# Performance work log

Measured on AMD Instinct MI355X. Metric: run time of the kernel, lower is better.

## Reference

```python
import jax, jax.numpy as jnp
import numpy as np

INP = 512
HIDDEN = 512
N_HEADS = 8          # called 'head_dim' in the torch code
D_HEAD = HIDDEN // N_HEADS  # 64
BASE = 10000.0
SCALE = D_HEAD ** (-0.5)


def rope(x):
    # x: [b, s, h, d]
    b, s, h, d = x.shape
    half = d // 2
    theta = 1.0 / (BASE ** (jnp.arange(0, d, 2, dtype=jnp.float32) / d))  # [d/2]
    idx_theta = jnp.arange(s, dtype=jnp.float32)[:, None] * theta[None, :]  # [s, d/2]
    idx_theta2 = jnp.concatenate([idx_theta, idx_theta], axis=1)            # [s, d]
    neg_half = jnp.concatenate([-x[..., half:], x[..., :half]], axis=-1)
    cos = jnp.cos(idx_theta2)[None, :, None, :]
    sin = jnp.sin(idx_theta2)[None, :, None, :]
    return x * cos + neg_half * sin


def setup_inputs() -> dict:
    key = jax.random.key(0)
    ks = jax.random.split(key, 10)
    b, s = 4, 2048
    init = lambda k, shp, fan_in: jax.random.normal(k, shp, jnp.float32) * (fan_in ** -0.5)
    return {
        "x": jax.random.normal(ks[0], (b, s, INP), jnp.float32),
        "c": jax.random.normal(ks[1], (b, s, INP), jnp.float32),
        "Wq": init(ks[2], (INP, HIDDEN), INP), "bq": jnp.zeros((HIDDEN,), jnp.float32),
        "Wk": init(ks[3], (INP, HIDDEN), INP), "bk": jnp.zeros((HIDDEN,), jnp.float32),
        "Wv": init(ks[4], (INP, HIDDEN), INP), "bv": jnp.zeros((HIDDEN,), jnp.float32),
        "Wo": init(ks[5], (HIDDEN, INP), HIDDEN), "bo": jnp.zeros((INP,), jnp.float32),
    }


def reference(x, c, Wq, bq, Wk, bk, Wv, bv, Wo, bo):
    b, s, _ = x.shape
    h_res = x
    q = (c @ Wq + bq).reshape(b, s, N_HEADS, D_HEAD)
    k = (x @ Wk + bk).reshape(b, s, N_HEADS, D_HEAD)
    v = (x @ Wv + bv).reshape(b, s, N_HEADS, D_HEAD)
    q = rope(q)
    k = rope(k)  # computed but unused, exactly as in the source
    # NOTE: source computes scores between q and V (not k) -- faithful reproduction
    att = jnp.einsum('bihd,bjhd->bhij', q, v)            # [b, h, s, s]
    att = jax.nn.softmax(att * SCALE, axis=-1)
    out = jnp.einsum('bhij,bjhd->bihd', att, v)          # [b, s, h, d]
    out = out.reshape(b, s, HIDDEN)
    out = out @ Wo + bo
    return out + h_res
```

## Files before the change

kernel.cpp:

```cpp
#include <hip/hip_runtime.h>
#include <hip/hip_bf16.h>
#include <cstdint>

typedef float f32x4 __attribute__((ext_vector_type(4)));
typedef float f32x16 __attribute__((ext_vector_type(16)));
typedef short bf16x8 __attribute__((ext_vector_type(8)));
typedef short bf16x4 __attribute__((ext_vector_type(4)));
typedef unsigned int u32x2 __attribute__((ext_vector_type(2)));
typedef unsigned short u16;

#define B_    4
#define S_    2048
#define H_    8
#define D_    64
#define M_    8192

#define OFF_CBF   0UL
#define OFF_XBF   8388608UL
#define OFF_QBH   16777216UL
#define OFF_VBH   25165824UL
#define OFF_VTBH  33554432UL
#define OFF_ATTN  41943040UL
#define OFF_WQT   50331648UL
#define OFF_WVT   50855936UL
#define OFF_WOT   51380224UL
#define OFF_BIAS  51904512UL
#define OFF_COS   51910656UL
#define OFF_SIN   52172800UL
#define WS_NEEDED 52434944UL

__device__ __forceinline__ u16 f2bf(float f){
    union { float f; uint32_t u; } v; v.f = f;
    uint32_t r = (v.u + 0x7fffu + ((v.u >> 16) & 1u)) >> 16;
    return (u16)r;
}
__device__ __forceinline__ float bf2f(u16 h){
    union { uint32_t u; float f; } v; v.u = ((uint32_t)h) << 16;
    return v.f;
}

__device__ __forceinline__ uint32_t cvtpk(float lo, float hi){
    uint32_t r;
    asm("v_cvt_pk_bf16_f32 %0, %1, %2" : "=v"(r) : "v"(lo), "v"(hi));
    return r;
}
__device__ __forceinline__ void plswap(uint32_t &va, uint32_t &vb){
#if __has_builtin(__builtin_amdgcn_permlane32_swap)
    u32x2 r = __builtin_amdgcn_permlane32_swap(va, vb, false, false);
    va = r[0]; vb = r[1];
#else
    asm volatile("v_permlane32_swap_b32 %0, %1" : "+v"(va), "+v"(vb));
#endif
}

__device__ __forceinline__ f32x16 mfma32(bf16x8 a, bf16x8 b, f32x16 c){
    return __builtin_amdgcn_mfma_f32_32x32x16_bf16(a, b, c, 0, 0, 0);
}

__device__ __forceinline__ void deint(uint4 a, uint4 b, bf16x8 &lo, bf16x8 &hi){
    union { bf16x8 v; uint32_t d[4]; } L, H;
    uint32_t s0=a.x, s1=a.y, s2=a.z, s3=a.w, s4=b.x, s5=b.y, s6=b.z, s7=b.w;
    L.d[0] = (s0 & 0xffffu) | (s1 << 16);
    L.d[1] = (s2 & 0xffffu) | (s3 << 16);
    L.d[2] = (s4 & 0xffffu) | (s5 << 16);
    L.d[3] = (s6 & 0xffffu) | (s7 << 16);
    H.d[0] = (s0 >> 16) | (s1 & 0xffff0000u);
    H.d[1] = (s2 >> 16) | (s3 & 0xffff0000u);
    H.d[2] = (s4 >> 16) | (s5 & 0xffff0000u);
    H.d[3] = (s6 >> 16) | (s7 & 0xffff0000u);
    lo = L.v; hi = H.v;
}

__device__ __forceinline__ int swz(int row, int col){
    return (col & ~63) | ((((col >> 3) & 7) ^ (row & 7)) << 3) | (col & 7);
}

__device__ __forceinline__ int detect_f32(const void* x_in){
    int lane = threadIdx.x & 63;
    ushort2 dv = ((const ushort2*)x_in)[lane];
    bool hit = ((((dv.x >> 7) & 0xFF) >= 160) || (((dv.y >> 7) & 0xFF) >= 160));
    return __ballot(hit) != 0ULL;
}

__device__ __forceinline__ void gload_lds16(const u16* g, u16* l){
    __builtin_amdgcn_global_load_lds(
        (const __attribute__((address_space(1))) void*)g,
        (__attribute__((address_space(3))) void*)l, 16, 0, 0);
}

__global__ void k_prep(const void* c_in, const void* x_in,
                       const void* Wq, const void* Wv, const void* Wo,
                       const void* bq, const void* bv, const void* bo,
                       u16* c_bf, u16* x_bf,
                       u16* Wqt, u16* Wvt, u16* Wot, float* bias_ws,
                       float* cos_t, float* sin_t){
    int bid = blockIdx.x;
    if (bid >= 7168){
        int idx = (bid - 7168) * 256 + threadIdx.x;
        int pos = idx >> 5, j = idx & 31;
        double theta = pow(10000.0, -(double)j / 32.0);
        double rev = ((double)pos * theta) * 0.15915494309189535;
        rev -= floor(rev);
        float fr = (float)rev;
        cos_t[idx] = __builtin_amdgcn_cosf(fr);
        sin_t[idx] = __builtin_amdgcn_sinf(fr);
        return;
    }
    if (bid >= 4096){
        int f = detect_f32(x_in);
        int wi = (bid - 4096) >> 10;
        int idx = ((bid - 4096) & 1023) * 256 + threadIdx.x;
        int k = idx >> 9, n = idx & 511;
        const void* W; u16* Wt; const void* bb;
        if (wi == 0){ W = Wq; Wt = Wqt; bb = bq; }
        else if (wi == 1){ W = Wv; Wt = Wvt; bb = bv; }
        else { W = Wo; Wt = Wot; bb = bo; }
        float v = f ? ((const float*)W)[idx] : bf2f(((const u16*)W)[idx]);
        Wt[n * 512 + (wi == 2 ? k : swz(n, k))] = f2bf(v);
        if (idx < 512){
            float b = f ? ((const float*)bb)[idx] : bf2f(((const u16*)bb)[idx]);
            bias_ws[wi * 512 + idx] = b;
        }
        return;
    }
    int f = detect_f32(x_in);
    int isx = bid >= 2048;
    int t = (bid & 2047) * 256 + threadIdx.x;
    const void* src = isx ? x_in : c_in;
    u16* dst = isx ? x_bf : c_bf;
    int e0 = t * 8, row = e0 >> 9, col = e0 & 511;
    size_t didx = (size_t)row * 512 + swz(row, col);
    bf16x8 o;
    if (f){
        float4 lo = ((const float4*)src)[t*2];
        float4 hi = ((const float4*)src)[t*2 + 1];
        union { bf16x8 v; uint32_t d[4]; } u;
        u.d[0] = cvtpk(lo.x, lo.y); u.d[1] = cvtpk(lo.z, lo.w);
        u.d[2] = cvtpk(hi.x, hi.y); u.d[3] = cvtpk(hi.z, hi.w);
        o = u.v;
    } else {
        o = *(const bf16x8*)((const u16*)src + e0);
    }
    *(bf16x8*)(dst + didx) = o;
}

__global__ __launch_bounds__(256) void k_gemm_qv(
    const u16* __restrict__ c_bf, const u16* __restrict__ x_bf,
    const u16* __restrict__ Wqt, const u16* __restrict__ Wvt,
    const float* __restrict__ bias_ws,
    const float* __restrict__ cos_t, const float* __restrict__ sin_t,
    u16* __restrict__ Qbh, u16* __restrict__ Vbh, u16* __restrict__ Vtbh)
{
    __shared__ __align__(16) u16 Als[2][128 * 64];
    __shared__ __align__(16) u16 Bls[2][128 * 64];
    const int w = threadIdx.x >> 6, lane = threadIdx.x & 63;
    const int g = lane >> 4, cq = lane & 15;
    const int wm = w & 1, wn = w >> 1;
    const int z = blockIdx.z;
    const u16* A  = z ? x_bf : c_bf;
    const u16* Wt = z ? Wvt : Wqt;
    const float* bias = bias_ws + (z ? 512 : 0);
    const int m0b = blockIdx.x * 128, n0b = blockIdx.y * 128;
    const int m0 = m0b + wm * 64, n0 = n0b + wn * 64;
    const int swzi = ((cq & 7) << 3);

    int srow[4], scol[4];
    #pragma unroll
    for (int i = 0; i < 4; i++){
        int flat = (w * 4 + i) * 64 + lane;
        srow[i] = flat >> 3; scol[i] = (flat & 7) * 8;
    }

    const f32x4 zero = {0.f, 0.f, 0.f, 0.f};
    f32x4 acc[4][4];
    #pragma unroll
    for (int i = 0; i < 4; i++)
        #pragma unroll
        for (int j = 0; j < 4; j++) acc[i][j] = zero;

    #pragma unroll
    for (int i = 0; i < 4; i++){
        gload_lds16(A  + (size_t)(m0b + srow[i]) * 512 + scol[i], &Als[0][(w*4 + i) * 512]);
        gload_lds16(Wt + (size_t)(n0b + srow[i]) * 512 + scol[i], &Bls[0][(w*4 + i) * 512]);
    }

    for (int kt = 0; kt < 8; kt++){
        const int buf = kt & 1;
        __builtin_amdgcn_s_waitcnt(0x0F70);
        __syncthreads();
        if (kt < 7){
            const int kk = (kt + 1) * 64;
            #pragma unroll
            for (int i = 0; i < 4; i++){
                gload_lds16(A  + (size_t)(m0b + srow[i]) * 512 + kk + scol[i], &Als[buf^1][(w*4 + i) * 512]);
                gload_lds16(Wt + (size_t)(n0b + srow[i]) * 512 + kk + scol[i], &Bls[buf^1][(w*4 + i) * 512]);
            }
        }
        #pragma unroll
        for (int ks = 0; ks < 2; ks++){
            const int cs = ((ks * 4 + g) << 3) ^ swzi;
            bf16x8 a[4], b[4];
            #pragma unroll
            for (int mt = 0; mt < 4; mt++)
                a[mt] = *(const bf16x8*)&Als[buf][(wm*64 + mt*16 + cq) * 64 + cs];
            #pragma unroll
            for (int nt = 0; nt < 4; nt++)
                b[nt] = *(const bf16x8*)&Bls[buf][(wn*64 + nt*16 + cq) * 64 + cs];
            #pragma unroll
            for (int mt = 0; mt < 4; mt++)
                #pragma unroll
                for (int nt = 0; nt < 4; nt++)
                    acc[mt][nt] = __builtin_amdgcn_mfma_f32_16x16x32_bf16(a[mt], b[nt], acc[mt][nt], 0, 0, 0);
        }
    }
    __syncthreads();

    #pragma unroll
    for (int nt = 0; nt < 4; nt++){
        float bvv = bias[n0 + nt*16 + cq];
        #pragma unroll
        for (int mt = 0; mt < 4; mt++) acc[mt][nt] += bvv;
    }
    const int h = n0 >> 6;
    if (z == 0){
        const float SCL = 0.125f * 1.4426950408889634f;
        uint32_t* Qpk = (uint32_t*)Qbh;
        #pragma unroll
        for (int mt = 0; mt < 4; mt++){
            #pragma unroll
            for (int r = 0; r < 4; r++){
                int row = m0 + mt*16 + g*4 + r;
                int b_idx = row >> 11, si = row & 2047;
                size_t base = ((size_t)(b_idx*8 + h) * 2048 + si) * 32;
                #pragma unroll
                for (int nt = 0; nt < 2; nt++){
                    int dj = nt*16 + cq;
                    float cv = cos_t[si*32 + dj], sv = sin_t[si*32 + dj];
                    float x1 = acc[mt][nt][r], x2 = acc[mt][nt+2][r];
                    Qpk[base + dj] = cvtpk((x1*cv - x2*sv) * SCL, (x2*cv + x1*sv) * SCL);
                }
            }
        }
    } else {
        float* ltw = ((float*)&Als[0][0]) + w * (16 * 65);
        const int b_idx = m0 >> 11, si0 = m0 & 2047;
        const size_t tbase = ((size_t)(b_idx*8 + h) * 64) * 2048;
        #pragma unroll
        for (int mt = 0; mt < 4; mt++)
            #pragma unroll
            for (int r = 0; r < 4; r++){
                int row = m0 + mt*16 + g*4 + r;
                int bi = row >> 11, si = row & 2047;
                size_t base = ((size_t)(bi*8 + h) * 2048 + si) * 64;
                #pragma unroll
                for (int nt = 0; nt < 4; nt++)
                    Vbh[base + nt*16 + cq] = f2bf(acc[mt][nt][r]);
            }
        #pragma unroll
        for (int nt = 0; nt < 4; nt++){
            #pragma unroll
            for (int mt = 0; mt < 4; mt++)
                #pragma unroll
                for (int r = 0; r < 4; r++)
                    ltw[cq * 65 + mt*16 + g*4 + r] = acc[mt][nt][r];
            __builtin_amdgcn_wave_barrier();
            #pragma unroll
            for (int dd = 0; dd < 16; dd++){
                float v = ltw[dd * 65 + lane];
                Vtbh[tbase + (size_t)(nt*16 + dd) * 2048 + si0 + lane] = f2bf(v);
            }
            __builtin_amdgcn_wave_barrier();
        }
    }
}

__global__ __launch_bounds__(256, 2) void k_attn(
    const u16* __restrict__ Qbh, const u16* __restrict__ Vbh,
    const u16* __restrict__ Vtbh,
    u16* __restrict__ part0, u16* __restrict__ part1, float* __restrict__ lsum)
{
    __shared__ __align__(16) u16 Vs[2][64 * 68];
    __shared__ __align__(16) u16 Vts[2][64 * 68];

    const int bid = blockIdx.x;
    const int logical = (bid & 7) * 64 + (bid >> 3);
    const int xb = logical & 7;
    const int bh = (logical >> 3) & 31;
    const int z  = logical >> 8;

    const int w = threadIdx.x >> 6, lane = threadIdx.x & 63;
    const int r32 = lane & 31, hl = lane >> 5;
    const int i0 = xb * 256 + w * 64;
    const int j0 = z * 1024;

    const uint32_t* Qpk = (const uint32_t*)Qbh;
    bf16x8 aq[2][4];
    #pragma unroll
    for (int it = 0; it < 2; it++){
        size_t qb = ((size_t)bh*2048 + i0 + it*32 + r32)*32 + hl*8;
        uint4 a0 = *(const uint4*)&Qpk[qb];
        uint4 a1 = *(const uint4*)&Qpk[qb + 4];
        uint4 b0 = *(const uint4*)&Qpk[qb + 16];
        uint4 b1 = *(const uint4*)&Qpk[qb + 20];
        deint(a0, a1, aq[it][0], aq[it][2]);
        deint(b0, b1, aq[it][1], aq[it][3]);
    }

    const int sr = w * 16 + (lane >> 2), sc = (lane & 3) * 16;
    const u16* gvs = Vbh  + ((size_t)bh*2048 + j0 + sr) * 64 + sc;
    const u16* gvt = Vtbh + ((size_t)bh*64 + sr) * 2048 + j0 + sc;
    const int ls = sr * 68 + sc;

    {
        bf16x8 a0 = *(const bf16x8*)gvs,       a1 = *(const bf16x8*)(gvs + 8);
        bf16x8 b0 = *(const bf16x8*)gvt,       b1 = *(const bf16x8*)(gvt + 8);
        *(bf16x8*)&Vs[0][ls]  = a0;  *(bf16x8*)&Vs[0][ls + 8]  = a1;
        *(bf16x8*)&Vts[0][ls] = b0;  *(bf16x8*)&Vts[0][ls + 8] = b1;
    }

    f32x16 ot[2][2];
    #pragma unroll
    for (int it = 0; it < 2; it++)
        #pragma unroll
        for (int dt = 0; dt < 2; dt++)
            #pragma unroll
            for (int rr = 0; rr < 16; rr++) ot[it][dt][rr] = 0.f;
    const f32x16 zero16 = ot[0][0];
    float fl[2] = {0.f, 0.f};
    bf16x8 pb[2][4];

    {
        bf16x8 na0 = *(const bf16x8*)(gvs + 4096);
        bf16x8 na1 = *(const bf16x8*)(gvs + 4096 + 8);
        bf16x8 nb0 = *(const bf16x8*)(gvt + 64);
        bf16x8 nb1 = *(const bf16x8*)(gvt + 64 + 8);
        __syncthreads();
        #pragma unroll
        for (int jtile = 0; jtile < 2; jtile++){
            bf16x8 vf[4];
            #pragma unroll
            for (int kk = 0; kk < 4; kk++)
                vf[kk] = *(const bf16x8*)&Vs[0][(jtile*32 + r32)*68 + kk*16 + hl*8];
            f32x16 st0 = zero16, st1 = zero16;
            __builtin_amdgcn_s_setprio(1);
            #pragma unroll
            for (int kk = 0; kk < 4; kk++){
                st0 = mfma32(vf[kk], aq[0][kk], st0);
                st1 = mfma32(vf[kk], aq[1][kk], st1);
            }
            __builtin_amdgcn_s_setprio(0);
            #pragma unroll
            for (int rr = 0; rr < 16; rr++) st0[rr] = __builtin_amdgcn_exp2f(st0[rr]);
            #pragma unroll
            for (int rr = 0; rr < 16; rr++) st1[rr] = __builtin_amdgcn_exp2f(st1[rr]);
            fl[0] += ((st0[0]+st0[1])+(st0[2]+st0[3])) + ((st0[4]+st0[5])+(st0[6]+st0[7]))
                   + ((st0[8]+st0[9])+(st0[10]+st0[11])) + ((st0[12]+st0[13])+(st0[14]+st0[15]));
            fl[1] += ((st1[0]+st1[1])+(st1[2]+st1[3])) + ((st1[4]+st1[5])+(st1[6]+st1[7]))
                   + ((st1[8]+st1[9])+(st1[10]+st1[11])) + ((st1[12]+st1[13])+(st1[14]+st1[15]));
            #pragma unroll
            for (int c = 0; c < 2; c++){
                uint32_t dA1 = cvtpk(st0[c*8+0], st0[c*8+1]);
                uint32_t dA2 = cvtpk(st0[c*8+2], st0[c*8+3]);
                uint32_t dB1 = cvtpk(st0[c*8+4], st0[c*8+5]);
                uint32_t dB2 = cvtpk(st0[c*8+6], st0[c*8+7]);
                plswap(dA1, dB1); plswap(dA2, dB2);
                union { bf16x8 v; uint32_t d[4]; } u;
                u.d[0] = dA1; u.d[1] = dA2; u.d[2] = dB1; u.d[3] = dB2;
                pb[0][jtile*2 + c] = u.v;
            }
            #pragma unroll
            for (int c = 0; c < 2; c++){
                uint32_t dA1 = cvtpk(st1[c*8+0], st1[c*8+1]);
                uint32_t dA2 = cvtpk(st1[c*8+2], st1[c*8+3]);
                uint32_t dB1 = cvtpk(st1[c*8+4], st1[c*8+5]);
                uint32_t dB2 = cvtpk(st1[c*8+6], st1[c*8+7]);
                plswap(dA1, dB1); plswap(dA2, dB2);
                union { bf16x8 v; uint32_t d[4]; } u;
                u.d[0] = dA1; u.d[1] = dA2; u.d[2] = dB1; u.d[3] = dB2;
                pb[1][jtile*2 + c] = u.v;
            }
        }
        *(bf16x8*)&Vs[1][ls]  = na0;  *(bf16x8*)&Vs[1][ls + 8]  = na1;
        *(bf16x8*)&Vts[1][ls] = nb0;  *(bf16x8*)&Vts[1][ls + 8] = nb1;
    }

    for (int jt = 1; jt < 16; jt++){
        const int bufA = jt & 1, bufB = bufA ^ 1;
        __syncthreads();
        bf16x8 na0, na1, nb0, nb1;
        if (jt < 15){
            na0 = *(const bf16x8*)(gvs + (size_t)(jt + 1) * 4096);
            na1 = *(const bf16x8*)(gvs + (size_t)(jt + 1) * 4096 + 8);
            nb0 = *(const bf16x8*)(gvt + (size_t)(jt + 1) * 64);
            nb1 = *(const bf16x8*)(gvt + (size_t)(jt + 1) * 64 + 8);
        }
        #pragma unroll
        for (int jtile = 0; jtile < 2; jtile++){
            bf16x8 vf[4];
            #pragma unroll
            for (int kk = 0; kk < 4; kk++)
                vf[kk] = *(const bf16x8*)&Vs[bufA][(jtile*32 + r32)*68 + kk*16 + hl*8];
            f32x16 st0 = zero16, st1 = zero16;
            __builtin_amdgcn_s_setprio(1);
            #pragma unroll
            for (int kk = 0; kk < 4; kk++){
                st0 = mfma32(vf[kk], aq[0][kk], st0);
                st1 = mfma32(vf[kk], aq[1][kk], st1);
            }
            #pragma unroll
            for (int cc = 0; cc < 2; cc++){
                const int c = jtile*2 + cc;
                bf16x8 vt0 = *(const bf16x8*)&Vts[bufB][r32*68 + c*16 + hl*8];
                bf16x8 vt1 = *(const bf16x8*)&Vts[bufB][(32 + r32)*68 + c*16 + hl*8];
                ot[0][0] = mfma32(vt0, pb[0][c], ot[0][0]);
                ot[1][0] = mfma32(vt0, pb[1][c], ot[1][0]);
                ot[0][1] = mfma32(vt1, pb[0][c], ot[0][1]);
                ot[1][1] = mfma32(vt1, pb[1][c], ot[1][1]);
            }
            __builtin_amdgcn_s_setprio(0);
            #pragma unroll
            for (int rr = 0; rr < 16; rr++) st0[rr] = __builtin_amdgcn_exp2f(st0[rr]);
            #pragma unroll
            for (int rr = 0; rr < 16; rr++) st1[rr] = __builtin_amdgcn_exp2f(st1[rr]);
            fl[0] += ((st0[0]+st0[1])+(st0[2]+st0[3])) + ((st0[4]+st0[5])+(st0[6]+st0[7]))
                   + ((st0[8]+st0[9])+(st0[10]+st0[11])) + ((st0[12]+st0[13])+(st0[14]+st0[15]));
            fl[1] += ((st1[0]+st1[1])+(st1[2]+st1[3])) + ((st1[4]+st1[5])+(st1[6]+st1[7]))
                   + ((st1[8]+st1[9])+(st1[10]+st1[11])) + ((st1[12]+st1[13])+(st1[14]+st1[15]));
            #pragma unroll
            for (int c = 0; c < 2; c++){
                uint32_t dA1 = cvtpk(st0[c*8+0], st0[c*8+1]);
                uint32_t dA2 = cvtpk(st0[c*8+2], st0[c*8+3]);
                uint32_t dB1 = cvtpk(st0[c*8+4], st0[c*8+5]);
                uint32_t dB2 = cvtpk(st0[c*8+6], st0[c*8+7]);
                plswap(dA1, dB1); plswap(dA2, dB2);
                union { bf16x8 v; uint32_t d[4]; } u;
                u.d[0] = dA1; u.d[1] = dA2; u.d[2] = dB1; u.d[3] = dB2;
                pb[0][jtile*2 + c] = u.v;
            }
            #pragma unroll
            for (int c = 0; c < 2; c++){
                uint32_t dA1 = cvtpk(st1[c*8+0], st1[c*8+1]);
                uint32_t dA2 = cvtpk(st1[c*8+2], st1[c*8+3]);
                uint32_t dB1 = cvtpk(st1[c*8+4], st1[c*8+5]);
                uint32_t dB2 = cvtpk(st1[c*8+6], st1[c*8+7]);
                plswap(dA1, dB1); plswap(dA2, dB2);
                union { bf16x8 v; uint32_t d[4]; } u;
                u.d[0] = dA1; u.d[1] = dA2; u.d[2] = dB1; u.d[3] = dB2;
                pb[1][jtile*2 + c] = u.v;
            }
        }
        __syncthreads();
        if (jt < 15){
            *(bf16x8*)&Vs[bufB][ls]  = na0;  *(bf16x8*)&Vs[bufB][ls + 8]  = na1;
            *(bf16x8*)&Vts[bufB][ls] = nb0;  *(bf16x8*)&Vts[bufB][ls + 8] = nb1;
        }
    }

    __builtin_amdgcn_s_setprio(1);
    #pragma unroll
    for (int c = 0; c < 4; c++){
        bf16x8 vt0 = *(const bf16x8*)&Vts[1][r32*68 + c*16 + hl*8];
        bf16x8 vt1 = *(const bf16x8*)&Vts[1][(32 + r32)*68 + c*16 + hl*8];
        ot[0][0] = mfma32(vt0, pb[0][c], ot[0][0]);
        ot[1][0] = mfma32(vt0, pb[1][c], ot[1][0]);
        ot[0][1] = mfma32(vt1, pb[0][c], ot[0][1]);
        ot[1][1] = mfma32(vt1, pb[1][c], ot[1][1]);
    }
    __builtin_amdgcn_s_setprio(0);

    const int b_idx = bh >> 3, hh = bh & 7;
    u16* part = z ? part1 : part0;
    #pragma unroll
    for (int it = 0; it < 2; it++){
        float sum = fl[it] + __shfl_xor(fl[it], 32);
        const int row = b_idx*2048 + i0 + it*32 + r32;
        if (lane < 32)
            lsum[(size_t)z*65536 + (size_t)hh*8192 + row] = sum;
        #pragma unroll
        for (int dt = 0; dt < 2; dt++){
            #pragma unroll
            for (int q = 0; q < 4; q++){
                float v0 = ot[it][dt][q*4+0];
                float v1 = ot[it][dt][q*4+1];
                float v2 = ot[it][dt][q*4+2];
                float v3 = ot[it][dt][q*4+3];
                uint2 pw;
                pw.x = cvtpk(v0, v1);
                pw.y = cvtpk(v2, v3);
                int col = hh*64 + dt*32 + q*8 + hl*4;
                *(uint2*)&part[(size_t)row * 512 + col] = pw;
            }
        }
    }
}

__global__ __launch_bounds__(256) void k_gemm_out(
    const u16* __restrict__ part0, const u16* __restrict__ part1,
    const float* __restrict__ lsum,
    const u16* __restrict__ Wot, const float* __restrict__ bias_ws,
    const void* __restrict__ x_in, void* __restrict__ out)
{
    __shared__ __align__(16) u16 Als[2][128 * 68];
    __shared__ __align__(16) u16 Bls[2][64 * 68];
    const int w = threadIdx.x >> 6, lane = threadIdx.x & 63;
    const int g = lane >> 4, cq = lane & 15;
    const int wm = w & 1, wn = w >> 1;
    const int m0b = blockIdx.x * 128, n0b = blockIdx.y * 64;
    const int m0 = m0b + wm * 64, n0 = n0b + wn * 32;
    const int f = detect_f32(x_in);

    int sra[4], sca[4], srb[2], scb[2];
    #pragma unroll
    for (int i = 0; i < 4; i++){
        int flat = (w * 4 + i) * 64 + lane;
        sra[i] = flat >> 3; sca[i] = (flat & 7) * 8;
    }
    #pragma unroll
    for (int i = 0; i < 2; i++){
        int flat = (w * 2 + i) * 64 + lane;
        srb[i] = flat >> 3; scb[i] = (flat & 7) * 8;
    }

    const f32x4 zero = {0.f, 0.f, 0.f, 0.f};
    f32x4 acc[4][2];
    #pragma unroll
    for (int i = 0; i < 4; i++)
        #pragma unroll
        for (int j = 0; j < 2; j++) acc[i][j] = zero;

    bf16x8 pa0[4], pa1[4], pb[2]; float pr[4];
    #pragma unroll
    for (int i = 0; i < 4; i++){
        int row = m0b + sra[i];
        pa0[i] = *(const bf16x8*)&part0[(size_t)row * 512 + sca[i]];
        pa1[i] = *(const bf16x8*)&part1[(size_t)row * 512 + sca[i]];
        pr[i] = 1.f / (lsum[row] + lsum[65536 + row]);
    }
    #pragma unroll
    for (int i = 0; i < 2; i++)
        pb[i] = *(const bf16x8*)&Wot[(size_t)(n0b + srb[i]) * 512 + scb[i]];
    #pragma unroll
    for (int i = 0; i < 4; i++){
        union { bf16x8 v; u16 e[8]; } a8;
        #pragma unroll
        for (int e = 0; e < 8; e++)
            a8.e[e] = f2bf((bf2f((u16)pa0[i][e]) + bf2f((u16)pa1[i][e])) * pr[i]);
        *(bf16x8*)&Als[0][sra[i]*68 + sca[i]] = a8.v;
    }
    #pragma unroll
    for (int i = 0; i < 2; i++)
        *(bf16x8*)&Bls[0][srb[i]*68 + scb[i]] = pb[i];

    for (int kt = 0; kt < 8; kt++){
        const int buf = kt & 1;
        __syncthreads();
        if (kt < 7){
            const int kk = (kt + 1) * 64, h = kt + 1;
            #pragma unroll
            for (int i = 0; i < 4; i++){
                int row = m0b + sra[i];
                pa0[i] = *(const bf16x8*)&part0[(size_t)row * 512 + kk + sca[i]];
                pa1[i] = *(const bf16x8*)&part1[(size_t)row * 512 + kk + sca[i]];
                pr[i] = 1.f / (lsum[(size_t)h*8192 + row] + lsum[65536 + (size_t)h*8192 + row]);
            }
            #pragma unroll
            for (int i = 0; i < 2; i++)
                pb[i] = *(const bf16x8*)&Wot[(size_t)(n0b + srb[i]) * 512 + kk + scb[i]];
        }
        #pragma unroll
        for (int ks = 0; ks < 2; ks++){
            bf16x8 a[4], b[2];
            #pragma unroll
            for (int mt = 0; mt < 4; mt++)
                a[mt] = *(const bf16x8*)&Als[buf][(wm*64 + mt*16 + cq)*68 + ks*32 + g*8];
            #pragma unroll
            for (int nt = 0; nt < 2; nt++)
                b[nt] = *(const bf16x8*)&Bls[buf][(wn*32 + nt*16 + cq)*68 + ks*32 + g*8];
            #pragma unroll
            for (int mt = 0; mt < 4; mt++)
                #pragma unroll
                for (int nt = 0; nt < 2; nt++)
                    acc[mt][nt] = __builtin_amdgcn_mfma_f32_16x16x32_bf16(a[mt], b[nt], acc[mt][nt], 0, 0, 0);
        }
        if (kt < 7){
            #pragma unroll
            for (int i = 0; i < 4; i++){
                union { bf16x8 v; u16 e[8]; } a8;
                #pragma unroll
                for (int e = 0; e < 8; e++)
                    a8.e[e] = f2bf((bf2f((u16)pa0[i][e]) + bf2f((u16)pa1[i][e])) * pr[i]);
                *(bf16x8*)&Als[buf^1][sra[i]*68 + sca[i]] = a8.v;
            }
            #pragma unroll
            for (int i = 0; i < 2; i++)
                *(bf16x8*)&Bls[buf^1][srb[i]*68 + scb[i]] = pb[i];
        }
    }
    #pragma unroll
    for (int mt = 0; mt < 4; mt++)
        #pragma unroll
        for (int nt = 0; nt < 2; nt++)
            #pragma unroll
            for (int r = 0; r < 4; r++){
                int row = m0 + mt*16 + g*4 + r;
                int col = n0 + nt*16 + cq;
                size_t idx = (size_t)row * 512 + col;
                float resid = f ? ((const float*)x_in)[idx] : bf2f(((const u16*)x_in)[idx]);
                float v = acc[mt][nt][r] + bias_ws[1024 + col] + resid;
                if (f) ((float*)out)[idx] = v;
                else   ((u16*)out)[idx] = f2bf(v);
            }
}

extern "C" void kernel_launch(void* const* d_in, const int* in_sizes, int n_in,
                              void* d_out, int out_size, void* d_ws, size_t ws_size,
                              hipStream_t stream){
    const void* x_in = d_in[0];
    const void* c_in = d_in[1];
    const void* Wq = d_in[2]; const void* bq = d_in[3];
    const void* Wv = d_in[6]; const void* bv = d_in[7];
    const void* Wo = d_in[8]; const void* bo = d_in[9];

    if (ws_size < WS_NEEDED){
        hipMemsetAsync(d_out, 0, (size_t)out_size * 2, stream);
        return;
    }
    char* ws = (char*)d_ws;
    u16* c_bf  = (u16*)(ws + OFF_CBF);
    u16* x_bf  = (u16*)(ws + OFF_XBF);
    u16* Qbh   = (u16*)(ws + OFF_QBH);
    u16* Vbh   = (u16*)(ws + OFF_VBH);
    u16* Vtbh  = (u16*)(ws + OFF_VTBH);
    u16* part0 = (u16*)(ws + OFF_ATTN);
    u16* part1 = (u16*)(ws + OFF_CBF);
    float* lsum = (float*)(ws + OFF_XBF);
    u16* Wqt   = (u16*)(ws + OFF_WQT);
    u16* Wvt   = (u16*)(ws + OFF_WVT);
    u16* Wot   = (u16*)(ws + OFF_WOT);
    float* bias_ws = (float*)(ws + OFF_BIAS);
    float* cos_t   = (float*)(ws + OFF_COS);
    float* sin_t   = (float*)(ws + OFF_SIN);

    k_prep<<<7424, 256, 0, stream>>>(c_in, x_in, Wq, Wv, Wo, bq, bv, bo,
                                     c_bf, x_bf, Wqt, Wvt, Wot, bias_ws, cos_t, sin_t);
    k_gemm_qv<<<dim3(64, 4, 2), 256, 0, stream>>>(c_bf, x_bf, Wqt, Wvt, bias_ws,
                                                  cos_t, sin_t, Qbh, Vbh, Vtbh);
    k_attn<<<dim3(512), 256, 0, stream>>>(Qbh, Vbh, Vtbh, part0, part1, lsum);
    k_gemm_out<<<dim3(64, 8), 256, 0, stream>>>(part0, part1, lsum, Wot, bias_ws,
                                                x_in, d_out);
}
```

Measured before the change: 181.7 us.

## Halve attention query rows per wave and double grid for occupancy

```diff
diff --git a/kernel.cpp b/kernel.cpp
--- a/kernel.cpp
+++ b/kernel.cpp
@@ -274,7 +274,7 @@
     }
 }
 
-__global__ __launch_bounds__(256, 2) void k_attn(
+__global__ __launch_bounds__(256, 4) void k_attn(
     const u16* __restrict__ Qbh, const u16* __restrict__ Vbh,
     const u16* __restrict__ Vtbh,
     u16* __restrict__ part0, u16* __restrict__ part1, float* __restrict__ lsum)
@@ -283,27 +283,26 @@
     __shared__ __align__(16) u16 Vts[2][64 * 68];
 
     const int bid = blockIdx.x;
-    const int logical = (bid & 7) * 64 + (bid >> 3);
-    const int xb = logical & 7;
-    const int bh = (logical >> 3) & 31;
-    const int z  = logical >> 8;
+    const int logical = (bid & 7) * 128 + (bid >> 3);
+    const int xb = logical & 15;
+    const int bh = (logical >> 4) & 31;
+    const int z  = logical >> 9;
 
     const int w = threadIdx.x >> 6, lane = threadIdx.x & 63;
     const int r32 = lane & 31, hl = lane >> 5;
-    const int i0 = xb * 256 + w * 64;
+    const int i0 = xb * 128 + w * 32;
     const int j0 = z * 1024;
 
     const uint32_t* Qpk = (const uint32_t*)Qbh;
-    bf16x8 aq[2][4];
-    #pragma unroll
-    for (int it = 0; it < 2; it++){
-        size_t qb = ((size_t)bh*2048 + i0 + it*32 + r32)*32 + hl*8;
+    bf16x8 aq[4];
+    {
+        size_t qb = ((size_t)bh*2048 + i0 + r32)*32 + hl*8;
         uint4 a0 = *(const uint4*)&Qpk[qb];
         uint4 a1 = *(const uint4*)&Qpk[qb + 4];
         uint4 b0 = *(const uint4*)&Qpk[qb + 16];
         uint4 b1 = *(const uint4*)&Qpk[qb + 20];
-        deint(a0, a1, aq[it][0], aq[it][2]);
-        deint(b0, b1, aq[it][1], aq[it][3]);
+        deint(a0, a1, aq[0], aq[2]);
+        deint(b0, b1, aq[1], aq[3]);
     }
 
     const int sr = w * 16 + (lane >> 2), sc = (lane & 3) * 16;
@@ -318,16 +317,14 @@
         *(bf16x8*)&Vts[0][ls] = b0;  *(bf16x8*)&Vts[0][ls + 8] = b1;
     }
 
-    f32x16 ot[2][2];
-    #pragma unroll
-    for (int it = 0; it < 2; it++)
-        #pragma unroll
-        for (int dt = 0; dt < 2; dt++)
-            #pragma unroll
-            for (int rr = 0; rr < 16; rr++) ot[it][dt][rr] = 0.f;
-    const f32x16 zero16 = ot[0][0];
-    float fl[2] = {0.f, 0.f};
-    bf16x8 pb[2][4];
+    f32x16 ot[2];
+    #pragma unroll
+    for (int dt = 0; dt < 2; dt++)
+        #pragma unroll
+        for (int rr = 0; rr < 16; rr++) ot[dt][rr] = 0.f;
+    const f32x16 zero16 = ot[0];
+    float fl = 0.f;
+    bf16x8 pb[4];
 
     {
         bf16x8 na0 = *(const bf16x8*)(gvs + 4096);
@@ -341,43 +338,26 @@
             #pragma unroll
             for (int kk = 0; kk < 4; kk++)
                 vf[kk] = *(const bf16x8*)&Vs[0][(jtile*32 + r32)*68 + kk*16 + hl*8];
-            f32x16 st0 = zero16, st1 = zero16;
+            f32x16 st = zero16;
             __builtin_amdgcn_s_setprio(1);
             #pragma unroll
-            for (int kk = 0; kk < 4; kk++){
-                st0 = mfma32(vf[kk], aq[0][kk], st0);
-                st1 = mfma32(vf[kk], aq[1][kk], st1);
-            }
+            for (int kk = 0; kk < 4; kk++)
+                st = mfma32(vf[kk], aq[kk], st);
             __builtin_amdgcn_s_setprio(0);
             #pragma unroll
-            for (int rr = 0; rr < 16; rr++) st0[rr] = __builtin_amdgcn_exp2f(st0[rr]);
-            #pragma unroll
-            for (int rr = 0; rr < 16; rr++) st1[rr] = __builtin_amdgcn_exp2f(st1[rr]);
-            fl[0] += ((st0[0]+st0[1])+(st0[2]+st0[3])) + ((st0[4]+st0[5])+(st0[6]+st0[7]))
-                   + ((st0[8]+st0[9])+(st0[10]+st0[11])) + ((st0[12]+st0[13])+(st0[14]+st0[15]));
-            fl[1] += ((st1[0]+st1[1])+(st1[2]+st1[3])) + ((st1[4]+st1[5])+(st1[6]+st1[7]))
-                   + ((st1[8]+st1[9])+(st1[10]+st1[11])) + ((st1[12]+st1[13])+(st1[14]+st1[15]));
+            for (int rr = 0; rr < 16; rr++) st[rr] = __builtin_amdgcn_exp2f(st[rr]);
+            fl += ((st[0]+st[1])+(st[2]+st[3])) + ((st[4]+st[5])+(st[6]+st[7]))
+                + ((st[8]+st[9])+(st[10]+st[11])) + ((st[12]+st[13])+(st[14]+st[15]));
             #pragma unroll
             for (int c = 0; c < 2; c++){
-                uint32_t dA1 = cvtpk(st0[c*8+0], st0[c*8+1]);
-                uint32_t dA2 = cvtpk(st0[c*8+2], st0[c*8+3]);
-                uint32_t dB1 = cvtpk(st0[c*8+4], st0[c*8+5]);
-                uint32_t dB2 = cvtpk(st0[c*8+6], st0[c*8+7]);
+                uint32_t dA1 = cvtpk(st[c*8+0], st[c*8+1]);
+                uint32_t dA2 = cvtpk(st[c*8+2], st[c*8+3]);
+                uint32_t dB1 = cvtpk(st[c*8+4], st[c*8+5]);
+                uint32_t dB2 = cvtpk(st[c*8+6], st[c*8+7]);
                 plswap(dA1, dB1); plswap(dA2, dB2);
                 union { bf16x8 v; uint32_t d[4]; } u;
                 u.d[0] = dA1; u.d[1] = dA2; u.d[2] = dB1; u.d[3] = dB2;
-                pb[0][jtile*2 + c] = u.v;
-            }
-            #pragma unroll
-            for (int c = 0; c < 2; c++){
-                uint32_t dA1 = cvtpk(st1[c*8+0], st1[c*8+1]);
-                uint32_t dA2 = cvtpk(st1[c*8+2], st1[c*8+3]);
-                uint32_t dB1 = cvtpk(st1[c*8+4], st1[c*8+5]);
-                uint32_t dB2 = cvtpk(st1[c*8+6], st1[c*8+7]);
-                plswap(dA1, dB1); plswap(dA2, dB2);
-                union { bf16x8 v; uint32_t d[4]; } u;
-                u.d[0] = dA1; u.d[1] = dA2; u.d[2] = dB1; u.d[3] = dB2;
-                pb[1][jtile*2 + c] = u.v;
+                pb[jtile*2 + c] = u.v;
             }
         }
         *(bf16x8*)&Vs[1][ls]  = na0;  *(bf16x8*)&Vs[1][ls + 8]  = na1;
@@ -400,53 +380,34 @@
             #pragma unroll
             for (int kk = 0; kk < 4; kk++)
                 vf[kk] = *(const bf16x8*)&Vs[bufA][(jtile*32 + r32)*68 + kk*16 + hl*8];
-            f32x16 st0 = zero16, st1 = zero16;
+            f32x16 st = zero16;
             __builtin_amdgcn_s_setprio(1);
             #pragma unroll
-            for (int kk = 0; kk < 4; kk++){
-                st0 = mfma32(vf[kk], aq[0][kk], st0);
-                st1 = mfma32(vf[kk], aq[1][kk], st1);
-            }
+            for (int kk = 0; kk < 4; kk++)
+                st = mfma32(vf[kk], aq[kk], st);
             #pragma unroll
             for (int cc = 0; cc < 2; cc++){
                 const int c = jtile*2 + cc;
                 bf16x8 vt0 = *(const bf16x8*)&Vts[bufB][r32*68 + c*16 + hl*8];
                 bf16x8 vt1 = *(const bf16x8*)&Vts[bufB][(32 + r32)*68 + c*16 + hl*8];
-                ot[0][0] = mfma32(vt0, pb[0][c], ot[0][0]);
-                ot[1][0] = mfma32(vt0, pb[1][c], ot[1][0]);
-                ot[0][1] = mfma32(vt1, pb[0][c], ot[0][1]);
-                ot[1][1] = mfma32(vt1, pb[1][c], ot[1][1]);
+                ot[0] = mfma32(vt0, pb[c], ot[0]);
+                ot[1] = mfma32(vt1, pb[c], ot[1]);
             }
             __builtin_amdgcn_s_setprio(0);
             #pragma unroll
-            for (int rr = 0; rr < 16; rr++) st0[rr] = __builtin_amdgcn_exp2f(st0[rr]);
-            #pragma unroll
-            for (int rr = 0; rr < 16; rr++) st1[rr] = __builtin_amdgcn_exp2f(st1[rr]);
-            fl[0] += ((st0[0]+st0[1])+(st0[2]+st0[3])) + ((st0[4]+st0[5])+(st0[6]+st0[7]))
-                   + ((st0[8]+st0[9])+(st0[10]+st0[11])) + ((st0[12]+st0[13])+(st0[14]+st0[15]));
-            fl[1] += ((st1[0]+st1[1])+(st1[2]+st1[3])) + ((st1[4]+st1[5])+(st1[6]+st1[7]))
-                   + ((st1[8]+st1[9])+(st1[10]+st1[11])) + ((st1[12]+st1[13])+(st1[14]+st1[15]));
+            for (int rr = 0; rr < 16; rr++) st[rr] = __builtin_amdgcn_exp2f(st[rr]);
+            fl += ((st[0]+st[1])+(st[2]+st[3])) + ((st[4]+st[5])+(st[6]+st[7]))
+                + ((st[8]+st[9])+(st[10]+st[11])) + ((st[12]+st[13])+(st[14]+st[15]));
             #pragma unroll
             for (int c = 0; c < 2; c++){
-                uint32_t dA1 = cvtpk(st0[c*8+0], st0[c*8+1]);
-                uint32_t dA2 = cvtpk(st0[c*8+2], st0[c*8+3]);
-                uint32_t dB1 = cvtpk(st0[c*8+4], st0[c*8+5]);
-                uint32_t dB2 = cvtpk(st0[c*8+6], st0[c*8+7]);
+                uint32_t dA1 = cvtpk(st[c*8+0], st[c*8+1]);
+                uint32_t dA2 = cvtpk(st[c*8+2], st[c*8+3]);
+                uint32_t dB1 = cvtpk(st[c*8+4], st[c*8+5]);
+                uint32_t dB2 = cvtpk(st[c*8+6], st[c*8+7]);
                 plswap(dA1, dB1); plswap(dA2, dB2);
                 union { bf16x8 v; uint32_t d[4]; } u;
                 u.d[0] = dA1; u.d[1] = dA2; u.d[2] = dB1; u.d[3] = dB2;
-                pb[0][jtile*2 + c] = u.v;
-            }
-            #pragma unroll
-            for (int c = 0; c < 2; c++){
-                uint32_t dA1 = cvtpk(st1[c*8+0], st1[c*8+1]);
-                uint32_t dA2 = cvtpk(st1[c*8+2], st1[c*8+3]);
-                uint32_t dB1 = cvtpk(st1[c*8+4], st1[c*8+5]);
-                uint32_t dB2 = cvtpk(st1[c*8+6], st1[c*8+7]);
-                plswap(dA1, dB1); plswap(dA2, dB2);
-                union { bf16x8 v; uint32_t d[4]; } u;
-                u.d[0] = dA1; u.d[1] = dA2; u.d[2] = dB1; u.d[3] = dB2;
-                pb[1][jtile*2 + c] = u.v;
+                pb[jtile*2 + c] = u.v;
             }
         }
         __syncthreads();
@@ -461,29 +422,26 @@
     for (int c = 0; c < 4; c++){
         bf16x8 vt0 = *(const bf16x8*)&Vts[1][r32*68 + c*16 + hl*8];
         bf16x8 vt1 = *(const bf16x8*)&Vts[1][(32 + r32)*68 + c*16 + hl*8];
-        ot[0][0] = mfma32(vt0, pb[0][c], ot[0][0]);
-        ot[1][0] = mfma32(vt0, pb[1][c], ot[1][0]);
-        ot[0][1] = mfma32(vt1, pb[0][c], ot[0][1]);
-        ot[1][1] = mfma32(vt1, pb[1][c], ot[1][1]);
+        ot[0] = mfma32(vt0, pb[c], ot[0]);
+        ot[1] = mfma32(vt1, pb[c], ot[1]);
     }
     __builtin_amdgcn_s_setprio(0);
 
     const int b_idx = bh >> 3, hh = bh & 7;
     u16* part = z ? part1 : part0;
-    #pragma unroll
-    for (int it = 0; it < 2; it++){
-        float sum = fl[it] + __shfl_xor(fl[it], 32);
-        const int row = b_idx*2048 + i0 + it*32 + r32;
+    {
+        float sum = fl + __shfl_xor(fl, 32);
+        const int row = b_idx*2048 + i0 + r32;
         if (lane < 32)
             lsum[(size_t)z*65536 + (size_t)hh*8192 + row] = sum;
         #pragma unroll
         for (int dt = 0; dt < 2; dt++){
             #pragma unroll
             for (int q = 0; q < 4; q++){
-                float v0 = ot[it][dt][q*4+0];
-                float v1 = ot[it][dt][q*4+1];
-                float v2 = ot[it][dt][q*4+2];
-                float v3 = ot[it][dt][q*4+3];
+                float v0 = ot[dt][q*4+0];
+                float v1 = ot[dt][q*4+1];
+                float v2 = ot[dt][q*4+2];
+                float v3 = ot[dt][q*4+3];
                 uint2 pw;
                 pw.x = cvtpk(v0, v1);
                 pw.y = cvtpk(v2, v3);
@@ -645,7 +603,7 @@
                                      c_bf, x_bf, Wqt, Wvt, Wot, bias_ws, cos_t, sin_t);
     k_gemm_qv<<<dim3(64, 4, 2), 256, 0, stream>>>(c_bf, x_bf, Wqt, Wvt, bias_ws,
                                                   cos_t, sin_t, Qbh, Vbh, Vtbh);
-    k_attn<<<dim3(512), 256, 0, stream>>>(Qbh, Vbh, Vtbh, part0, part1, lsum);
+    k_attn<<<dim3(1024), 256, 0, stream>>>(Qbh, Vbh, Vtbh, part0, part1, lsum);
     k_gemm_out<<<dim3(64, 8), 256, 0, stream>>>(part0, part1, lsum, Wot, bias_ws,
                                                 x_in, d_out);
 }
```

Result: slower. 186.5 us (+2.6%).
